# Kernel optimization log

Hardware: AMD Instinct MI355X
Metric: run time of the kernel (lower is better)

Reference implementation:

```python
import jax, jax.numpy as jnp
import numpy as np

BS, J, L, D = 32, 4, 512, 768  # batch, entity sentences, max_bert_len, bert_embed_dim
K = 4                          # num_entity_per_sentence; J*K == num_candidates == 16
OUT = 256                      # entity_final_output_dim


def setup_inputs() -> dict:
    key = jax.random.key(0)
    k1, k2, k3, k4 = jax.random.split(key, 4)
    zipped_entity = jax.random.normal(k1, (BS, J, L, D), dtype=jnp.float32)
    # strictly increasing separator indices per (b, j); spans are [last+1, sep)
    steps = jax.random.randint(k2, (BS, J, K), 5, 60)
    entity_token_sep_idx = 1 + jnp.cumsum(steps, axis=-1)  # values < 1+4*60 < L
    W = jax.random.normal(k3, (D, OUT), dtype=jnp.float32) * 0.02
    b = jax.random.normal(k4, (OUT,), dtype=jnp.float32) * 0.02
    return {"zipped_entity": zipped_entity,
            "entity_token_sep_idx": entity_token_sep_idx,
            "W": W, "b": b}


def reference(zipped_entity, entity_token_sep_idx, W, b):
    # Ragged per-entity span mean-pool, vectorized via a span mask, then Linear.
    sep = entity_token_sep_idx                                    # [bs, J, K]
    starts = jnp.concatenate([jnp.ones_like(sep[..., :1]), sep[..., :-1] + 1], axis=-1)
    ends = sep                                                    # exclusive
    t = jnp.arange(L)                                             # token positions
    # mask[b,j,k,l] = 1 if token l belongs to entity k of sentence j
    mask = ((t[None, None, None, :] >= starts[..., None]) &
            (t[None, None, None, :] < ends[..., None])).astype(zipped_entity.dtype)
    sums = jnp.einsum('bjkl,bjld->bjkd', mask, zipped_entity)     # [bs, J, K, D]
    counts = (ends - starts).astype(zipped_entity.dtype)[..., None]
    pooled = sums / counts                                        # mean over span
    bs = zipped_entity.shape[0]
    # entity_idx = k + j*K -> reshape [bs, J, K, D] to [bs, num_candidates, D]
    encoded_entity = pooled.reshape(bs, J * K, D)
    return encoded_entity @ W + b                                 # final Linear
```

## Files before the change

kernel.cpp:

```cpp
#include <hip/hip_runtime.h>
#include <hip/hip_bf16.h>

#define BS  32
#define J   4
#define L   512
#define D   768
#define K   4
#define OUT 256

typedef float f4 __attribute__((ext_vector_type(4)));

__global__ __launch_bounds__(256) void pool_kernel(
    const float* __restrict__ Z,
    const int*   __restrict__ sep,
    float*       __restrict__ ws)
{
    const int blk  = blockIdx.x;
    const int e    = blk >> 1, h = blk & 1;
    const int sent = e >> 2;
    const int k    = e & 3;
    const int end   = sep[sent * K + k];
    const int prev  = (k == 0) ? 0 : sep[sent * K + k - 1];
    const int start = prev + 1;
    const float inv = 1.0f / (float)(end - start);

    const int w    = threadIdx.x >> 6;
    const int lane = threadIdx.x & 63;
    const float* zbase = Z + (size_t)sent * L * D + lane * 4;

    f4 a0={0,0,0,0}, a1={0,0,0,0}, a2={0,0,0,0};
    f4 c0={0,0,0,0}, c1={0,0,0,0}, c2={0,0,0,0};

    int l = start + h + 2 * w;
    for (; l + 8 < end; l += 16) {
        const float* r0 = zbase + (size_t)l * D;
        const float* r1 = zbase + (size_t)(l + 8) * D;
        a0 += *(const f4*)(r0);       a1 += *(const f4*)(r0 + 256);
        a2 += *(const f4*)(r0 + 512);
        c0 += *(const f4*)(r1);       c1 += *(const f4*)(r1 + 256);
        c2 += *(const f4*)(r1 + 512);
    }
    if (l < end) {
        const float* r0 = zbase + (size_t)l * D;
        a0 += *(const f4*)(r0);       a1 += *(const f4*)(r0 + 256);
        a2 += *(const f4*)(r0 + 512);
    }
    a0 += c0; a1 += c1; a2 += c2;

    __shared__ float part[4][D];
    *(f4*)&part[w][lane*4]       = a0;
    *(f4*)&part[w][lane*4 + 256] = a1;
    *(f4*)&part[w][lane*4 + 512] = a2;
    __syncthreads();

    const int t = threadIdx.x;
    if (t < 192) {
        f4 s = {0,0,0,0};
        #pragma unroll
        for (int ww = 0; ww < 4; ++ww) s += *(const f4*)&part[ww][t*4];
        s *= inv;
        *(f4*)&ws[(((size_t)sent*2 + h)*K + k) * D + t*4] = s;
    }
}

__global__ __launch_bounds__(256) void gemm_kernel(
    const float* __restrict__ ws,
    const float* __restrict__ W,
    const float* __restrict__ bias,
    float*       __restrict__ out)
{
    const int g  = blockIdx.x >> 2;
    const int cq = blockIdx.x & 3;

    __shared__ float p[K * D];
    __shared__ float red[16][K][64];
    {
        const f4* a = (const f4*)(ws + (size_t)g * 2 * K * D);
        #pragma unroll
        for (int i = threadIdx.x; i < (K * D) / 4; i += 256) {
            f4 v = a[i] + a[i + (K * D) / 4];
            *(f4*)&p[i * 4] = v;
        }
    }
    __syncthreads();

    const int w    = threadIdx.x >> 6;
    const int lane = threadIdx.x & 63;
    const int dg   = lane >> 4;
    const int cl   = lane & 15;
    const int colbase = cq * 64 + cl * 4;
    const int dbase   = w * 192 + dg;

    f4 acc0={0,0,0,0}, acc1={0,0,0,0}, acc2={0,0,0,0}, acc3={0,0,0,0};
    #pragma unroll 4
    for (int i = 0; i < 48; ++i) {
        const int d = dbase + 4 * i;
        f4 wv = *(const f4*)&W[(size_t)d * OUT + colbase];
        acc0 += p[0 * D + d] * wv;
        acc1 += p[1 * D + d] * wv;
        acc2 += p[2 * D + d] * wv;
        acc3 += p[3 * D + d] * wv;
    }

    const int r = w * 4 + dg;
    *(f4*)&red[r][0][cl * 4] = acc0;
    *(f4*)&red[r][1][cl * 4] = acc1;
    *(f4*)&red[r][2][cl * 4] = acc2;
    *(f4*)&red[r][3][cl * 4] = acc3;
    __syncthreads();

    const int e2  = threadIdx.x >> 6;
    const int col = threadIdx.x & 63;
    float s = bias[cq * 64 + col];
    #pragma unroll
    for (int rr = 0; rr < 16; ++rr) s += red[rr][e2][col];
    out[(size_t)(g * K + e2) * OUT + cq * 64 + col] = s;
}

extern "C" void kernel_launch(void* const* d_in, const int* in_sizes, int n_in,
                              void* d_out, int out_size, void* d_ws, size_t ws_size,
                              hipStream_t stream) {
    const float* Z    = (const float*)d_in[0];
    const int*   sep  = (const int*)d_in[1];
    const float* W    = (const float*)d_in[2];
    const float* bias = (const float*)d_in[3];
    float*       out  = (float*)d_out;
    float*       ws   = (float*)d_ws;

    pool_kernel<<<2 * BS * J * K, 256, 0, stream>>>(Z, sep, ws);
    gemm_kernel<<<BS * J * K, 256, 0, stream>>>(ws, W, bias, out);
}
```

Baseline: 23.01 us.

## Split entity spans into quarters and schedule pool work via atomic work queue

Entity spans are now divided into four interleaved quarters instead of two, giving 2048 work units. Persistent-style blocks claim units from a global atomic counter rather than one block per unit, which balances load across ragged span lengths. The GEMM kernel now sums four partial vectors per entity instead of two. This adds a memset launch, an atomic per unit and extra synchronisation, and it drops the two-row unrolling in the inner load loop.

```diff
diff --git a/kernel.cpp b/kernel.cpp
--- a/kernel.cpp
+++ b/kernel.cpp
@@ -7,59 +7,60 @@
 #define D   768
 #define K   4
 #define OUT 256
+#define NUNITS (4 * BS * J * K)
 
 typedef float f4 __attribute__((ext_vector_type(4)));
 
 __global__ __launch_bounds__(256) void pool_kernel(
     const float* __restrict__ Z,
     const int*   __restrict__ sep,
-    float*       __restrict__ ws)
+    float*       __restrict__ ws,
+    int*         __restrict__ ctr)
 {
-    const int blk  = blockIdx.x;
-    const int e    = blk >> 1, h = blk & 1;
-    const int sent = e >> 2;
-    const int k    = e & 3;
-    const int end   = sep[sent * K + k];
-    const int prev  = (k == 0) ? 0 : sep[sent * K + k - 1];
-    const int start = prev + 1;
-    const float inv = 1.0f / (float)(end - start);
+    __shared__ float part[4][D];
+    __shared__ int   s_unit;
 
-    const int w    = threadIdx.x >> 6;
-    const int lane = threadIdx.x & 63;
-    const float* zbase = Z + (size_t)sent * L * D + lane * 4;
+    const int tid  = threadIdx.x;
+    const int w    = tid >> 6;
+    const int lane = tid & 63;
 
-    f4 a0={0,0,0,0}, a1={0,0,0,0}, a2={0,0,0,0};
-    f4 c0={0,0,0,0}, c1={0,0,0,0}, c2={0,0,0,0};
+    for (;;) {
+        if (tid == 0)
+            s_unit = __hip_atomic_fetch_add(ctr, 1, __ATOMIC_RELAXED,
+                                            __HIP_MEMORY_SCOPE_AGENT);
+        __syncthreads();
+        const int u = s_unit;
+        if (u >= NUNITS) return;
 
-    int l = start + h + 2 * w;
-    for (; l + 8 < end; l += 16) {
-        const float* r0 = zbase + (size_t)l * D;
-        const float* r1 = zbase + (size_t)(l + 8) * D;
-        a0 += *(const f4*)(r0);       a1 += *(const f4*)(r0 + 256);
-        a2 += *(const f4*)(r0 + 512);
-        c0 += *(const f4*)(r1);       c1 += *(const f4*)(r1 + 256);
-        c2 += *(const f4*)(r1 + 512);
-    }
-    if (l < end) {
-        const float* r0 = zbase + (size_t)l * D;
-        a0 += *(const f4*)(r0);       a1 += *(const f4*)(r0 + 256);
-        a2 += *(const f4*)(r0 + 512);
-    }
-    a0 += c0; a1 += c1; a2 += c2;
+        const int e    = u >> 2, q = u & 3;
+        const int sent = e >> 2, k = e & 3;
+        const int end   = sep[sent * K + k];
+        const int prev  = (k == 0) ? 0 : sep[sent * K + k - 1];
+        const int start = prev + 1;
+        const float inv = 1.0f / (float)(end - start);
+        const float* zbase = Z + (size_t)sent * L * D + lane * 4;
 
-    __shared__ float part[4][D];
-    *(f4*)&part[w][lane*4]       = a0;
-    *(f4*)&part[w][lane*4 + 256] = a1;
-    *(f4*)&part[w][lane*4 + 512] = a2;
-    __syncthreads();
+        f4 a0 = {0,0,0,0}, a1 = {0,0,0,0}, a2 = {0,0,0,0};
+        for (int l = start + q + 4 * w; l < end; l += 16) {
+            const float* r = zbase + (size_t)l * D;
+            a0 += *(const f4*)(r);
+            a1 += *(const f4*)(r + 256);
+            a2 += *(const f4*)(r + 512);
+        }
 
-    const int t = threadIdx.x;
-    if (t < 192) {
-        f4 s = {0,0,0,0};
-        #pragma unroll
-        for (int ww = 0; ww < 4; ++ww) s += *(const f4*)&part[ww][t*4];
-        s *= inv;
-        *(f4*)&ws[(((size_t)sent*2 + h)*K + k) * D + t*4] = s;
+        *(f4*)&part[w][lane*4]       = a0;
+        *(f4*)&part[w][lane*4 + 256] = a1;
+        *(f4*)&part[w][lane*4 + 512] = a2;
+        __syncthreads();
+
+        if (tid < 192) {
+            f4 s = {0,0,0,0};
+            #pragma unroll
+            for (int ww = 0; ww < 4; ++ww) s += *(const f4*)&part[ww][tid*4];
+            s *= inv;
+            *(f4*)&ws[((size_t)e * 4 + q) * D + tid*4] = s;
+        }
+        __syncthreads();
     }
 }
 
@@ -75,10 +76,12 @@
     __shared__ float p[K * D];
     __shared__ float red[16][K][64];
     {
-        const f4* a = (const f4*)(ws + (size_t)g * 2 * K * D);
-        #pragma unroll
-        for (int i = threadIdx.x; i < (K * D) / 4; i += 256) {
-            f4 v = a[i] + a[i + (K * D) / 4];
+        const f4* a = (const f4*)(ws + (size_t)g * K * 4 * D);
+        for (int i = threadIdx.x; i < K * 192; i += 256) {
+            const int e2 = i / 192;
+            const int t  = i - e2 * 192;
+            const f4* base = a + (size_t)(e2 * 4) * 192;
+            f4 v = base[t] + base[t + 192] + base[t + 2*192] + base[t + 3*192];
             *(f4*)&p[i * 4] = v;
         }
     }
@@ -126,7 +129,9 @@
     const float* bias = (const float*)d_in[3];
     float*       out  = (float*)d_out;
     float*       ws   = (float*)d_ws;
+    int*         ctr  = (int*)(ws + (size_t)512 * 4 * D);
 
-    pool_kernel<<<2 * BS * J * K, 256, 0, stream>>>(Z, sep, ws);
+    hipMemsetAsync(ctr, 0, sizeof(int), stream);
+    pool_kernel<<<2 * BS * J * K, 256, 0, stream>>>(Z, sep, ws, ctr);
     gemm_kernel<<<BS * J * K, 256, 0, stream>>>(ws, W, bias, out);
 }
```

Result: slower. 57.45 us (+149.7%).
